# Kernel optimization log

Hardware: AMD Instinct MI355X
Metric: run time of the kernel (lower is better)

## Reference

```python
import jax, jax.numpy as jnp
import numpy as np

B, T, C, H = 8, 1024, 1024, 16
HD = C // H  # head dim = 64
NEG = -1e9


def setup_inputs() -> dict:
    key = jax.random.key(0)
    ks = jax.random.split(key, 10)
    total = B * T
    x = jax.random.normal(ks[0], (total, C), dtype=jnp.float32)
    # identity pack: each padded row is a contiguous chunk of tokens
    padpack_index = jnp.arange(total, dtype=jnp.int64).reshape(B, T)
    # sorted per-row sequence ids -> block-diagonal attention within each packed row
    padpack_batch = jnp.sort(jax.random.randint(ks[1], (B, T), 0, 4, dtype=jnp.int32), axis=-1)
    padpack_inverse_index = jnp.arange(total, dtype=jnp.int64)
    s = 1.0 / np.sqrt(C)
    Wq = jax.random.uniform(ks[2], (C, C), jnp.float32, -s, s)
    bq = jax.random.uniform(ks[3], (C,), jnp.float32, -s, s)
    Wk = jax.random.uniform(ks[4], (C, C), jnp.float32, -s, s)
    bk = jax.random.uniform(ks[5], (C,), jnp.float32, -s, s)
    Wv = jax.random.uniform(ks[6], (C, C), jnp.float32, -s, s)
    bv = jax.random.uniform(ks[7], (C,), jnp.float32, -s, s)
    Wp = jax.random.uniform(ks[8], (C, C), jnp.float32, -s, s)
    bp = jax.random.uniform(ks[9], (C,), jnp.float32, -s, s)
    return {"x": x, "padpack_index": padpack_index, "padpack_batch": padpack_batch,
            "padpack_inverse_index": padpack_inverse_index,
            "Wq": Wq, "bq": bq, "Wk": Wk, "bk": bk, "Wv": Wv, "bv": bv, "Wp": Wp, "bp": bp}


def reference(x, padpack_index, padpack_batch, padpack_inverse_index,
              Wq, bq, Wk, bk, Wv, bv, Wp, bp):
    # gather ragged tokens into padded [B, T, C]
    xp = x[padpack_index]
    # torch Linear: y = x @ W.T + b
    q = (xp @ Wq.T + bq).reshape(B, T, H, HD)
    k = (xp @ Wk.T + bk).reshape(B, T, H, HD)
    v = (xp @ Wv.T + bv).reshape(B, T, H, HD)
    scale = 1.0 / np.sqrt(HD).astype(np.float32)
    att = jnp.einsum('bihd,bjhd->bhij', q, k) * scale  # [B,H,T,T]
    # mask: token pairs from different packed sequences cannot attend
    mask = (padpack_batch[:, :, None] != padpack_batch[:, None, :])[:, None]  # [B,1,T,T]
    att = jnp.where(mask, NEG, att)
    att = jax.nn.softmax(att, axis=-1)
    y = jnp.einsum('bhij,bjhd->bihd', att, v).reshape(B, T, C)
    y = y @ Wp.T + bp
    # scatter back to ragged layout [total_tokens, C]
    return y.reshape(B * T, C)[padpack_inverse_index]
```

## Files before the change

kernel.cpp:

```cpp
#include <hip/hip_runtime.h>


typedef __attribute__((ext_vector_type(8))) short short8;
typedef __attribute__((ext_vector_type(4))) float f32x4;
typedef __attribute__((ext_vector_type(4))) unsigned uint4v;

#define MFMA16(a, b, c) __builtin_amdgcn_mfma_f32_16x16x32_bf16((a), (b), (c), 0, 0, 0)

__device__ __forceinline__ ushort f2b(float f) {
  union { float f; unsigned u; } v; v.f = f;
  unsigned u = v.u;
  return (ushort)((u + 0x7fffu + ((u >> 16) & 1u)) >> 16);
}

__device__ __forceinline__ void gload16(const void* g, void* l) {
  __builtin_amdgcn_global_load_lds((const __attribute__((address_space(1))) unsigned int*)g,
                                   (__attribute__((address_space(3))) unsigned int*)l,
                                   16, 0, 0);
}

__device__ __forceinline__ void cvt4(const float* __restrict__ s, ushort* __restrict__ d) {
  const float4 v = *(const float4*)s;
  ushort4 r; r.x = f2b(v.x); r.y = f2b(v.y); r.z = f2b(v.z); r.w = f2b(v.w);
  *(ushort4*)d = r;
}

__global__ __launch_bounds__(256) void prep(const float* __restrict__ x,
    const float* __restrict__ wq, const float* __restrict__ wk,
    const float* __restrict__ wv, const float* __restrict__ wp,
    ushort* __restrict__ xb, ushort* __restrict__ wb,
    const int* __restrict__ pb, int* __restrict__ bnd) {
  const int bid = blockIdx.x;
  if (bid >= 12288) {
    const int b = bid - 12288;
    const int* p = pb + b * 1024;
    const int i = threadIdx.x;
#pragma unroll
    for (int e = 0; e < 4; ++e) {
      const int idx = i * 4 + e;
      const int cur = p[idx];
      const int prev = (idx == 0) ? -1 : p[idx - 1];
      for (int v = prev + 1; v <= cur; ++v) bnd[b * 8 + v] = idx;
    }
    if (i == 255) {
      const int cur = p[1023];
      for (int v = cur + 1; v <= 4; ++v) bnd[b * 8 + v] = 1024;
    }
    return;
  }
  const long long e0 = ((long long)bid * 256 + threadIdx.x) * 4;
  const long long NX = 8388608ll;
  if (e0 < NX) {
    cvt4(x + e0, xb + e0);
  } else {
    const long long t = e0 - NX;
    const int sel = (int)(t >> 20);
    const float* w = sel == 0 ? wq : sel == 1 ? wk : sel == 2 ? wv : wp;
    cvt4(w + (t & 1048575), wb + t);
  }
}

template <int MODE>
__global__ __launch_bounds__(512, 2) void gemm8(
    const ushort* __restrict__ A, const ushort* __restrict__ Bw,
    const float* __restrict__ bias0, const float* __restrict__ bias1,
    const float* __restrict__ bias2,
    ushort* __restrict__ O0, ushort* __restrict__ O1, ushort* __restrict__ O2,
    float* __restrict__ Of) {
  constexpr int ACH = 256 * 64;
  constexpr int BCH = 128 * 64;
  constexpr int BUFB = 2 * (ACH + BCH);
  __shared__ __align__(16) char smem[3 * BUFB];

  const int tid = threadIdx.x, lane = tid & 63, wid = tid >> 6;
  const int wr = wid >> 1, wc = wid & 1;
  const int lg = lane >> 4, lc = lane & 15;

  const int id = blockIdx.x;
  const int s = id >> 3;
  const int m0 = ((id & 7) * 4 + (s & 3)) << 8;
  const int n0 = (s >> 2) << 7;

  f32x4 acc[4][4] = {};

  const int sr0 = tid >> 2;
  const int sc0 = (tid & 3) ^ ((sr0 >> 1) & 3);

#define STAGE(dst_, kh, kt) { \
    char* ad = (dst_) + (kh) * ACH; \
    char* bd = (dst_) + 2 * ACH + (kh) * BCH; \
    const int kcol = (kt) * 64 + (kh) * 32; \
    gload16(A + (size_t)(m0 + sr0) * 1024 + kcol + sc0 * 8, ad + tid * 16); \
    gload16(A + (size_t)(m0 + 128 + sr0) * 1024 + kcol + sc0 * 8, ad + (tid + 512) * 16); \
    gload16(Bw + (size_t)(n0 + sr0) * 1024 + kcol + sc0 * 8, bd + tid * 16); \
  }

#define PHASE_COMPUTE(src_, kh) { \
    const char* ab = (src_) + (kh) * ACH; \
    const char* bb = (src_) + 2 * ACH + (kh) * BCH; \
    short8 af[4]; short8 bf[4]; \
    _Pragma("unroll") \
    for (int f = 0; f < 4; ++f) { \
      const int row = wr * 64 + f * 16 + lc; \
      af[f] = *(const short8*)(ab + row * 64 + ((lg ^ ((row >> 1) & 3)) << 4)); \
    } \
    _Pragma("unroll") \
    for (int g = 0; g < 4; ++g) { \
      const int row = wc * 64 + g * 16 + lc; \
      bf[g] = *(const short8*)(bb + row * 64 + ((lg ^ ((row >> 1) & 3)) << 4)); \
    } \
    __builtin_amdgcn_s_setprio(1); \
    _Pragma("unroll") \
    for (int f = 0; f < 4; ++f) \
      _Pragma("unroll") \
      for (int g = 0; g < 4; ++g) \
        acc[f][g] = MFMA16(af[f], bf[g], acc[f][g]); \
    __builtin_amdgcn_s_setprio(0); \
  }

#define WAITVM(n) { asm volatile("s_waitcnt vmcnt(" #n ")" ::: "memory"); }
#define BARF() { __builtin_amdgcn_s_barrier(); asm volatile("" ::: "memory"); }

  char* b0 = smem;
  char* b1 = smem + BUFB;
  char* b2 = smem + 2 * BUFB;

  STAGE(b0, 0, 0)
  STAGE(b0, 1, 0)
  STAGE(b1, 0, 1)
  STAGE(b1, 1, 1)

  for (int t = 0; t < 14; ++t) {
    WAITVM(9)
    BARF()
    STAGE(b2, 0, t + 2)
    PHASE_COMPUTE(b0, 0)
    WAITVM(9)
    BARF()
    STAGE(b2, 1, t + 2)
    PHASE_COMPUTE(b0, 1)
    char* tmp = b0; b0 = b1; b1 = b2; b2 = tmp;
  }
  WAITVM(9)
  BARF()
  PHASE_COMPUTE(b0, 0)
  WAITVM(6)
  BARF()
  PHASE_COMPUTE(b0, 1)
  WAITVM(3)
  BARF()
  PHASE_COMPUTE(b1, 0)
  WAITVM(0)
  BARF()
  PHASE_COMPUTE(b1, 1)

  if constexpr (MODE == 0) {
    const int sel = n0 >> 10, nloc = n0 & 1023;
    const float* bias = sel == 0 ? bias0 : sel == 1 ? bias1 : bias2;
    float bval[4];
#pragma unroll
    for (int g = 0; g < 4; ++g) bval[g] = bias[nloc + wc * 64 + g * 16 + lc];
    if (sel < 2) {
      ushort* dst = sel ? O1 : O0;
#pragma unroll
      for (int f = 0; f < 4; ++f)
#pragma unroll
        for (int j = 0; j < 4; ++j) {
          const size_t row = m0 + wr * 64 + f * 16 + lg * 4 + j;
#pragma unroll
          for (int g = 0; g < 4; ++g)
            dst[row * 1024 + nloc + wc * 64 + g * 16 + lc] = f2b(acc[f][g][j] + bval[g]);
        }
    } else {
      ushort (*Ts)[136] = (ushort(*)[136])smem;
#pragma unroll
      for (int mh = 0; mh < 2; ++mh) {
        __syncthreads();
        if ((wr >> 1) == mh) {
#pragma unroll
          for (int f = 0; f < 4; ++f)
#pragma unroll
            for (int g = 0; g < 4; ++g)
#pragma unroll
              for (int j = 0; j < 4; ++j)
                Ts[(wr & 1) * 64 + f * 16 + lg * 4 + j][wc * 64 + g * 16 + lc] =
                    f2b(acc[f][g][j] + bval[g]);
        }
        __syncthreads();
        const int c = tid >> 2;
        const int th = (tid & 3) * 32;
        const int gt = m0 + mh * 128;
        const int b = gt >> 10;
        const int t0 = (gt & 1023) + th;
        const int gc = nloc + c;
        ushort* dp = O2 + ((size_t)((b * 16 + (gc >> 6)) * 64 + (gc & 63))) * 1024 + t0;
#pragma unroll
        for (int gb = 0; gb < 4; ++gb) {
          short8 pk;
#pragma unroll
          for (int u = 0; u < 8; ++u) pk[u] = (short)Ts[th + gb * 8 + u][c];
          *(short8*)(dp + gb * 8) = pk;
        }
      }
    }
  } else {
    float bval[4];
#pragma unroll
    for (int g = 0; g < 4; ++g) bval[g] = bias0[n0 + wc * 64 + g * 16 + lc];
#pragma unroll
    for (int f = 0; f < 4; ++f)
#pragma unroll
      for (int j = 0; j < 4; ++j) {
        const size_t row = m0 + wr * 64 + f * 16 + lg * 4 + j;
#pragma unroll
        for (int g = 0; g < 4; ++g)
          Of[row * 1024 + n0 + wc * 64 + g * 16 + lc] = acc[f][g][j] + bval[g];
      }
  }
#undef STAGE
#undef PHASE_COMPUTE
#undef WAITVM
#undef BARF
}

__global__ __launch_bounds__(512) void attn(const ushort* __restrict__ Q,
    const ushort* __restrict__ K, const ushort* __restrict__ Vt,
    const int* __restrict__ bnd, ushort* __restrict__ O) {
  __shared__ __align__(16) char kvbuf[2][16384];

  const int tid = threadIdx.x, lane = tid & 63;
  const int lg = lane >> 4, lc = lane & 15;

  const int id = blockIdx.x;
  const int xcd = id & 7, slot = id >> 3;
  const int bh = xcd + 8 * (slot >> 3);
  const int qt = slot & 7;
  const int b = bh >> 4, h = bh & 15;
  const int q0 = qt * 128 + (tid >> 6) * 16;

  const int* bd = bnd + b * 8;
  const int b1 = bd[1], b2 = bd[2], b3 = bd[3], b4 = bd[4];
#define SEGID(k) (((k) >= b1) + ((k) >= b2) + ((k) >= b3) + ((k) >= b4))

  const int qid = SEGID(q0 + lc);
  int klo_l = (qid > 0) ? b1 : 0;
  klo_l = (qid > 1) ? b2 : klo_l;
  klo_l = (qid > 2) ? b3 : klo_l;
  int khi_l = (qid > 0) ? b2 : b1;
  khi_l = (qid > 1) ? b3 : khi_l;
  khi_l = (qid > 2) ? b4 : khi_l;

  const int bq_lo = SEGID(qt * 128), bq_hi = SEGID(qt * 128 + 127);
  unsigned am = 0;
#pragma unroll
  for (int jt = 0; jt < 16; ++jt) {
    const int tlo = SEGID(jt * 64), thi = SEGID(jt * 64 + 63);
    if (thi >= bq_lo && tlo <= bq_hi) am |= (1u << jt);
  }

  const ushort* qp = Q + (size_t)(b * 1024 + q0 + lc) * 1024 + h * 64 + lg * 8;
  const short8 qf0 = *(const short8*)qp;
  const short8 qf1 = *(const short8*)(qp + 32);

  const int r0 = tid >> 3;
  const int c16 = (tid & 7) ^ (r0 & 7);
  const ushort* Kg = K + (size_t)(b * 1024 + r0) * 1024 + h * 64 + c16 * 8;
  const ushort* Vg = Vt + (size_t)(bh * 64 + r0) * 1024 + c16 * 8;

#define STAGE(bufp, j) { \
    gload16(Kg + (size_t)(j) * 1024, (bufp) + tid * 16); \
    gload16(Vg + (j), (bufp) + 8192 + tid * 16); }

#define SOFF(r, ch) ((r) * 128 + ((((ch) ^ ((r) & 7))) << 4))

  float mr = -1e30f, lr = 0.f;
  f32x4 o[4] = {};

  unsigned rem = am;
  int jc = __builtin_ctz(rem) * 64;
  rem &= rem - 1;
  STAGE(kvbuf[0], jc)
  __syncthreads();
  int cur = 0;

  const int aA = ((lane & 16) << 3) + ((lane & 15) << 2);
  const int aB = aA + 64;
  const bool hi = (lane & 32) != 0;

  for (;;) {
    int jn = -1;
    if (rem) {
      jn = __builtin_ctz(rem) * 64;
      rem &= rem - 1;
      STAGE(kvbuf[cur ^ 1], jn)
    }
    const char* bufK = kvbuf[cur];
    const char* bufV = kvbuf[cur] + 8192;

    short8 kf[8];
#pragma unroll
    for (int n = 0; n < 4; ++n) {
      const int rr = n * 16 + lc;
      kf[2 * n] = *(const short8*)(bufK + SOFF(rr, lg));
      kf[2 * n + 1] = *(const short8*)(bufK + SOFF(rr, lg + 4));
    }
    f32x4 s[4];
    __builtin_amdgcn_s_setprio(1);
#pragma unroll
    for (int n = 0; n < 4; ++n) {
      f32x4 z = {};
      z = MFMA16(kf[2 * n], qf0, z);
      s[n] = MFMA16(kf[2 * n + 1], qf1, z);
    }
    __builtin_amdgcn_s_setprio(0);

#pragma unroll
    for (int n = 0; n < 4; ++n) {
      const int kk = jc + n * 16 + lg * 4;
#pragma unroll
      for (int r = 0; r < 4; ++r) {
        const bool ok = (kk + r >= klo_l) && (kk + r < khi_l);
        s[n][r] = ok ? s[n][r] * 0.125f : -1e9f;
      }
    }

    float rm = fmaxf(fmaxf(fmaxf(s[0][0], s[0][1]), fmaxf(s[0][2], s[0][3])),
                     fmaxf(fmaxf(fmaxf(s[1][0], s[1][1]), fmaxf(s[1][2], s[1][3])),
                           fmaxf(fmaxf(fmaxf(s[2][0], s[2][1]), fmaxf(s[2][2], s[2][3])),
                                 fmaxf(fmaxf(s[3][0], s[3][1]), fmaxf(s[3][2], s[3][3])))));
    rm = fmaxf(rm, __shfl_xor(rm, 16));
    rm = fmaxf(rm, __shfl_xor(rm, 32));
    float mn = mr;
    if (!__all(rm <= mr + 8.f)) {
      mn = fmaxf(mr, rm);
      const float sf = __expf(mr - mn);
      mr = mn;
      lr *= sf;
      const float s0 = __shfl(sf, lg * 4 + 0);
      const float s1 = __shfl(sf, lg * 4 + 1);
      const float s2 = __shfl(sf, lg * 4 + 2);
      const float s3 = __shfl(sf, lg * 4 + 3);
#pragma unroll
      for (int n = 0; n < 4; ++n) {
        o[n][0] *= s0; o[n][1] *= s1; o[n][2] *= s2; o[n][3] *= s3;
      }
    }
    float rs = 0.f;
#pragma unroll
    for (int n = 0; n < 4; ++n)
#pragma unroll
      for (int r = 0; r < 4; ++r) {
        const float p = __expf(s[n][r] - mn);
        s[n][r] = p; rs += p;
      }
    rs += __shfl_xor(rs, 16);
    rs += __shfl_xor(rs, 32);
    lr += rs;

    unsigned u[4][2];
#pragma unroll
    for (int n = 0; n < 4; ++n) {
      asm("v_cvt_pk_bf16_f32 %0, %1, %2" : "=v"(u[n][0]) : "v"(s[n][0]), "v"(s[n][1]));
      asm("v_cvt_pk_bf16_f32 %0, %1, %2" : "=v"(u[n][1]) : "v"(s[n][2]), "v"(s[n][3]));
    }
    uint4v pwm[2];
#pragma unroll
    for (int m = 0; m < 2; ++m) {
      const unsigned x0 = __builtin_amdgcn_ds_bpermute(aA, u[2 * m][0]);
      const unsigned y0 = __builtin_amdgcn_ds_bpermute(aA, u[2 * m + 1][0]);
      const unsigned x1 = __builtin_amdgcn_ds_bpermute(aA, u[2 * m][1]);
      const unsigned y1 = __builtin_amdgcn_ds_bpermute(aA, u[2 * m + 1][1]);
      const unsigned x2 = __builtin_amdgcn_ds_bpermute(aB, u[2 * m][0]);
      const unsigned y2 = __builtin_amdgcn_ds_bpermute(aB, u[2 * m + 1][0]);
      const unsigned x3 = __builtin_amdgcn_ds_bpermute(aB, u[2 * m][1]);
      const unsigned y3 = __builtin_amdgcn_ds_bpermute(aB, u[2 * m + 1][1]);
      uint4v w;
      w.x = hi ? y0 : x0;
      w.y = hi ? y1 : x1;
      w.z = hi ? y2 : x2;
      w.w = hi ? y3 : x3;
      pwm[m] = w;
    }
    const short8 p0 = *reinterpret_cast<const short8*>(&pwm[0]);
    const short8 p1 = *reinterpret_cast<const short8*>(&pwm[1]);

    short8 vv[8];
#pragma unroll
    for (int n = 0; n < 4; ++n) {
      const int rr = n * 16 + lc;
      vv[2 * n] = *(const short8*)(bufV + SOFF(rr, lg));
      vv[2 * n + 1] = *(const short8*)(bufV + SOFF(rr, lg + 4));
    }
    __builtin_amdgcn_s_setprio(1);
#pragma unroll
    for (int n = 0; n < 4; ++n) {
      o[n] = MFMA16(p0, vv[2 * n], o[n]);
      o[n] = MFMA16(p1, vv[2 * n + 1], o[n]);
    }
    __builtin_amdgcn_s_setprio(0);

    if (jn < 0) break;
    __syncthreads();
    cur ^= 1;
    jc = jn;
  }

  const float linv = 1.f / lr;
  const float i0 = __shfl(linv, lg * 4 + 0);
  const float i1 = __shfl(linv, lg * 4 + 1);
  const float i2 = __shfl(linv, lg * 4 + 2);
  const float i3 = __shfl(linv, lg * 4 + 3);
#pragma unroll
  for (int n = 0; n < 4; ++n) {
    const size_t base = (size_t)(b * 1024 + q0) * 1024 + h * 64 + n * 16 + lc;
    O[base + 0 * 1024 + (size_t)lg * 4096] = f2b(o[n][0] * i0);
    O[base + 1 * 1024 + (size_t)lg * 4096] = f2b(o[n][1] * i1);
    O[base + 2 * 1024 + (size_t)lg * 4096] = f2b(o[n][2] * i2);
    O[base + 3 * 1024 + (size_t)lg * 4096] = f2b(o[n][3] * i3);
  }
#undef STAGE
#undef SOFF
#undef SEGID
}

extern "C" void kernel_launch(void* const* d_in, const int* in_sizes, int n_in,
                              void* d_out, int out_size, void* d_ws, size_t ws_size,
                              hipStream_t stream) {
  const float* x  = (const float*)d_in[0];
  const int*  pb  = (const int*)d_in[2];
  const float* Wq = (const float*)d_in[4]; const float* bq = (const float*)d_in[5];
  const float* Wk = (const float*)d_in[6]; const float* bk = (const float*)d_in[7];
  const float* Wv = (const float*)d_in[8]; const float* bv = (const float*)d_in[9];
  const float* Wp = (const float*)d_in[10]; const float* bp = (const float*)d_in[11];
  float* out = (float*)d_out;
  char* ws = (char*)d_ws;

  ushort* xb = (ushort*)ws;
  ushort* wb = (ushort*)(ws + (16u << 20));
  ushort* Qb = (ushort*)(ws + (24u << 20));
  ushort* Kb = (ushort*)(ws + (40u << 20));
  ushort* Vt = (ushort*)(ws + (56u << 20));
  int*    bnd = (int*)(ws + (72u << 20));
  ushort* Ob = xb;

  prep<<<12296, 256, 0, stream>>>(x, Wq, Wk, Wv, Wp, xb, wb, pb, bnd);
  gemm8<0><<<768, 512, 0, stream>>>(xb, wb, bq, bk, bv, Qb, Kb, Vt, nullptr);
  attn<<<1024, 512, 0, stream>>>(Qb, Kb, Vt, bnd, Ob);
  gemm8<1><<<256, 512, 0, stream>>>(Ob, wb + (3 << 20), bp,
                                    nullptr, nullptr, nullptr, nullptr, nullptr, out);
}
```

Measured before the change: 149.9 us.

## Process two KV tiles per attention loop iteration with larger LDS buffers

The attention kernel now stages and processes two 64-key tiles per loop iteration (128 keys), doubling the LDS double-buffer to 32KB per stage. Online-softmax max/rescale and the barrier happen once per pair of tiles instead of per tile, reducing synchronization and reduction overhead. Invalid second tiles are masked via a validity flag. It costs more LDS (64KB total) and registers, which may reduce occupancy, and odd tile counts waste a masked tile's compute.

After: 152.3 us. Within noise of the previous version (+1.6%).

```diff
diff --git a/kernel.cpp b/kernel.cpp
--- a/kernel.cpp
+++ b/kernel.cpp
@@ -226,7 +226,7 @@
 __global__ __launch_bounds__(512) void attn(const ushort* __restrict__ Q,
     const ushort* __restrict__ K, const ushort* __restrict__ Vt,
     const int* __restrict__ bnd, ushort* __restrict__ O) {
-  __shared__ __align__(16) char kvbuf[2][16384];
+  __shared__ __align__(16) char kvbuf[2][32768];
 
   const int tid = threadIdx.x, lane = tid & 63;
   const int lg = lane >> 4, lc = lane & 15;
@@ -267,7 +267,7 @@
   const ushort* Kg = K + (size_t)(b * 1024 + r0) * 1024 + h * 64 + c16 * 8;
   const ushort* Vg = Vt + (size_t)(bh * 64 + r0) * 1024 + c16 * 8;
 
-#define STAGE(bufp, j) { \
+#define STG1(bufp, j) { \
     gload16(Kg + (size_t)(j) * 1024, (bufp) + tid * 16); \
     gload16(Vg + (j), (bufp) + 8192 + tid * 16); }
 
@@ -277,9 +277,11 @@
   f32x4 o[4] = {};
 
   unsigned rem = am;
-  int jc = __builtin_ctz(rem) * 64;
-  rem &= rem - 1;
-  STAGE(kvbuf[0], jc)
+  int jA = __builtin_ctz(rem) * 64; rem &= rem - 1;
+  int jB = jA; bool vB = false;
+  if (rem) { jB = __builtin_ctz(rem) * 64; rem &= rem - 1; vB = true; }
+  STG1(kvbuf[0], jA)
+  STG1(kvbuf[0] + 16384, jB)
   __syncthreads();
   int cur = 0;
 
@@ -288,46 +290,70 @@
   const bool hi = (lane & 32) != 0;
 
   for (;;) {
-    int jn = -1;
+    int jA2 = -1, jB2 = 0; bool vB2 = false;
     if (rem) {
-      jn = __builtin_ctz(rem) * 64;
-      rem &= rem - 1;
-      STAGE(kvbuf[cur ^ 1], jn)
-    }
-    const char* bufK = kvbuf[cur];
-    const char* bufV = kvbuf[cur] + 8192;
-
-    short8 kf[8];
+      jA2 = __builtin_ctz(rem) * 64; rem &= rem - 1;
+      jB2 = jA2;
+      if (rem) { jB2 = __builtin_ctz(rem) * 64; rem &= rem - 1; vB2 = true; }
+      STG1(kvbuf[cur ^ 1], jA2)
+      STG1(kvbuf[cur ^ 1] + 16384, jB2)
+    }
+    const char* bA = kvbuf[cur];
+    const char* bB = kvbuf[cur] + 16384;
+
+    f32x4 s[8];
+    {
+      short8 kf[8];
+#pragma unroll
+      for (int n = 0; n < 4; ++n) {
+        const int rr = n * 16 + lc;
+        kf[2 * n] = *(const short8*)(bA + SOFF(rr, lg));
+        kf[2 * n + 1] = *(const short8*)(bA + SOFF(rr, lg + 4));
+      }
+      __builtin_amdgcn_s_setprio(1);
+#pragma unroll
+      for (int n = 0; n < 4; ++n) {
+        f32x4 z = {};
+        z = MFMA16(kf[2 * n], qf0, z);
+        s[n] = MFMA16(kf[2 * n + 1], qf1, z);
+      }
+      __builtin_amdgcn_s_setprio(0);
+    }
+    {
+      short8 kf[8];
+#pragma unroll
+      for (int n = 0; n < 4; ++n) {
+        const int rr = n * 16 + lc;
+        kf[2 * n] = *(const short8*)(bB + SOFF(rr, lg));
+        kf[2 * n + 1] = *(const short8*)(bB + SOFF(rr, lg + 4));
+      }
+      __builtin_amdgcn_s_setprio(1);
+#pragma unroll
+      for (int n = 0; n < 4; ++n) {
+        f32x4 z = {};
+        z = MFMA16(kf[2 * n], qf0, z);
+        s[4 + n] = MFMA16(kf[2 * n + 1], qf1, z);
+      }
+      __builtin_amdgcn_s_setprio(0);
+    }
+
 #pragma unroll
     for (int n = 0; n < 4; ++n) {
-      const int rr = n * 16 + lc;
-      kf[2 * n] = *(const short8*)(bufK + SOFF(rr, lg));
-      kf[2 * n + 1] = *(const short8*)(bufK + SOFF(rr, lg + 4));
-    }
-    f32x4 s[4];
-    __builtin_amdgcn_s_setprio(1);
-#pragma unroll
-    for (int n = 0; n < 4; ++n) {
-      f32x4 z = {};
-      z = MFMA16(kf[2 * n], qf0, z);
-      s[n] = MFMA16(kf[2 * n + 1], qf1, z);
-    }
-    __builtin_amdgcn_s_setprio(0);
-
-#pragma unroll
-    for (int n = 0; n < 4; ++n) {
-      const int kk = jc + n * 16 + lg * 4;
+      const int kkA = jA + n * 16 + lg * 4;
+      const int kkB = jB + n * 16 + lg * 4;
 #pragma unroll
       for (int r = 0; r < 4; ++r) {
-        const bool ok = (kk + r >= klo_l) && (kk + r < khi_l);
-        s[n][r] = ok ? s[n][r] * 0.125f : -1e9f;
-      }
-    }
-
-    float rm = fmaxf(fmaxf(fmaxf(s[0][0], s[0][1]), fmaxf(s[0][2], s[0][3])),
-                     fmaxf(fmaxf(fmaxf(s[1][0], s[1][1]), fmaxf(s[1][2], s[1][3])),
-                           fmaxf(fmaxf(fmaxf(s[2][0], s[2][1]), fmaxf(s[2][2], s[2][3])),
-                                 fmaxf(fmaxf(s[3][0], s[3][1]), fmaxf(s[3][2], s[3][3])))));
+        const bool okA = (kkA + r >= klo_l) && (kkA + r < khi_l);
+        s[n][r] = okA ? s[n][r] * 0.125f : -1e9f;
+        const bool okB = vB && (kkB + r >= klo_l) && (kkB + r < khi_l);
+        s[4 + n][r] = okB ? s[4 + n][r] * 0.125f : -1e9f;
+      }
+    }
+
+    float rm = -1e30f;
+#pragma unroll
+    for (int n = 0; n < 8; ++n)
+      rm = fmaxf(rm, fmaxf(fmaxf(s[n][0], s[n][1]), fmaxf(s[n][2], s[n][3])));
     rm = fmaxf(rm, __shfl_xor(rm, 16));
     rm = fmaxf(rm, __shfl_xor(rm, 32));
     float mn = mr;
@@ -347,7 +373,7 @@
     }
     float rs = 0.f;
 #pragma unroll
-    for (int n = 0; n < 4; ++n)
+    for (int n = 0; n < 8; ++n)
 #pragma unroll
       for (int r = 0; r < 4; ++r) {
         const float p = __expf(s[n][r] - mn);
@@ -357,52 +383,56 @@
     rs += __shfl_xor(rs, 32);
     lr += rs;
 
-    unsigned u[4][2];
-#pragma unroll
-    for (int n = 0; n < 4; ++n) {
-      asm("v_cvt_pk_bf16_f32 %0, %1, %2" : "=v"(u[n][0]) : "v"(s[n][0]), "v"(s[n][1]));
-      asm("v_cvt_pk_bf16_f32 %0, %1, %2" : "=v"(u[n][1]) : "v"(s[n][2]), "v"(s[n][3]));
-    }
-    uint4v pwm[2];
-#pragma unroll
-    for (int m = 0; m < 2; ++m) {
-      const unsigned x0 = __builtin_amdgcn_ds_bpermute(aA, u[2 * m][0]);
-      const unsigned y0 = __builtin_amdgcn_ds_bpermute(aA, u[2 * m + 1][0]);
-      const unsigned x1 = __builtin_amdgcn_ds_bpermute(aA, u[2 * m][1]);
-      const unsigned y1 = __builtin_amdgcn_ds_bpermute(aA, u[2 * m + 1][1]);
-      const unsigned x2 = __builtin_amdgcn_ds_bpermute(aB, u[2 * m][0]);
-      const unsigned y2 = __builtin_amdgcn_ds_bpermute(aB, u[2 * m + 1][0]);
-      const unsigned x3 = __builtin_amdgcn_ds_bpermute(aB, u[2 * m][1]);
-      const unsigned y3 = __builtin_amdgcn_ds_bpermute(aB, u[2 * m + 1][1]);
-      uint4v w;
-      w.x = hi ? y0 : x0;
-      w.y = hi ? y1 : x1;
-      w.z = hi ? y2 : x2;
-      w.w = hi ? y3 : x3;
-      pwm[m] = w;
-    }
-    const short8 p0 = *reinterpret_cast<const short8*>(&pwm[0]);
-    const short8 p1 = *reinterpret_cast<const short8*>(&pwm[1]);
-
-    short8 vv[8];
-#pragma unroll
-    for (int n = 0; n < 4; ++n) {
-      const int rr = n * 16 + lc;
-      vv[2 * n] = *(const short8*)(bufV + SOFF(rr, lg));
-      vv[2 * n + 1] = *(const short8*)(bufV + SOFF(rr, lg + 4));
-    }
-    __builtin_amdgcn_s_setprio(1);
-#pragma unroll
-    for (int n = 0; n < 4; ++n) {
-      o[n] = MFMA16(p0, vv[2 * n], o[n]);
-      o[n] = MFMA16(p1, vv[2 * n + 1], o[n]);
-    }
-    __builtin_amdgcn_s_setprio(0);
-
-    if (jn < 0) break;
+#pragma unroll
+    for (int t2 = 0; t2 < 2; ++t2) {
+      unsigned u[4][2];
+#pragma unroll
+      for (int n = 0; n < 4; ++n) {
+        asm("v_cvt_pk_bf16_f32 %0, %1, %2" : "=v"(u[n][0]) : "v"(s[4 * t2 + n][0]), "v"(s[4 * t2 + n][1]));
+        asm("v_cvt_pk_bf16_f32 %0, %1, %2" : "=v"(u[n][1]) : "v"(s[4 * t2 + n][2]), "v"(s[4 * t2 + n][3]));
+      }
+      uint4v pwm[2];
+#pragma unroll
+      for (int m = 0; m < 2; ++m) {
+        const unsigned x0 = __builtin_amdgcn_ds_bpermute(aA, u[2 * m][0]);
+        const unsigned y0 = __builtin_amdgcn_ds_bpermute(aA, u[2 * m + 1][0]);
+        const unsigned x1 = __builtin_amdgcn_ds_bpermute(aA, u[2 * m][1]);
+        const unsigned y1 = __builtin_amdgcn_ds_bpermute(aA, u[2 * m + 1][1]);
+        const unsigned x2 = __builtin_amdgcn_ds_bpermute(aB, u[2 * m][0]);
+        const unsigned y2 = __builtin_amdgcn_ds_bpermute(aB, u[2 * m + 1][0]);
+        const unsigned x3 = __builtin_amdgcn_ds_bpermute(aB, u[2 * m][1]);
+        const unsigned y3 = __builtin_amdgcn_ds_bpermute(aB, u[2 * m + 1][1]);
+        uint4v w;
+        w.x = hi ? y0 : x0;
+        w.y = hi ? y1 : x1;
+        w.z = hi ? y2 : x2;
+        w.w = hi ? y3 : x3;
+        pwm[m] = w;
+      }
+      const short8 p0 = *reinterpret_cast<const short8*>(&pwm[0]);
+      const short8 p1 = *reinterpret_cast<const short8*>(&pwm[1]);
+
+      const char* bufV = (t2 ? bB : bA) + 8192;
+      short8 vv[8];
+#pragma unroll
+      for (int n = 0; n < 4; ++n) {
+        const int rr = n * 16 + lc;
+        vv[2 * n] = *(const short8*)(bufV + SOFF(rr, lg));
+        vv[2 * n + 1] = *(const short8*)(bufV + SOFF(rr, lg + 4));
+      }
+      __builtin_amdgcn_s_setprio(1);
+#pragma unroll
+      for (int n = 0; n < 4; ++n) {
+        o[n] = MFMA16(p0, vv[2 * n], o[n]);
+        o[n] = MFMA16(p1, vv[2 * n + 1], o[n]);
+      }
+      __builtin_amdgcn_s_setprio(0);
+    }
+
+    if (jA2 < 0) break;
     __syncthreads();
     cur ^= 1;
-    jc = jn;
+    jA = jA2; jB = jB2; vB = vB2;
   }
 
   const float linv = 1.f / lr;
@@ -418,7 +448,7 @@
     O[base + 2 * 1024 + (size_t)lg * 4096] = f2b(o[n][2] * i2);
     O[base + 3 * 1024 + (size_t)lg * 4096] = f2b(o[n][3] * i3);
   }
-#undef STAGE
+#undef STG1
 #undef SOFF
 #undef SEGID
 }
```

## Shrink GEMM tiles to 128x128 with 4-wave blocks and single-phase k-steps

Applied to the files above, without the earlier changes.

Replaces the 256x128-tile, 8-wave GEMM with a 128x128-tile, 4-wave GEMM. It uses 32-wide k-steps in a triple-buffered pipeline with 48KB of shared memory, and doubles the grid sizes for both the QKV and output projections. The V-transpose epilogue is simplified to a single pass over the 128-row tile. The goal is more blocks and better occupancy and load balance across CUs, especially for the smaller output projection. In exchange, each loaded byte gets less reuse and global traffic per FLOP goes up.

New measurement: 150.9 us. About the same (+0.7%).

```diff
diff --git a/kernel.cpp b/kernel.cpp
--- a/kernel.cpp
+++ b/kernel.cpp
@@ -61,43 +61,38 @@
 }
 
 template <int MODE>
-__global__ __launch_bounds__(512, 2) void gemm8(
+__global__ __launch_bounds__(256) void gemm4(
     const ushort* __restrict__ A, const ushort* __restrict__ Bw,
     const float* __restrict__ bias0, const float* __restrict__ bias1,
     const float* __restrict__ bias2,
     ushort* __restrict__ O0, ushort* __restrict__ O1, ushort* __restrict__ O2,
     float* __restrict__ Of) {
-  constexpr int ACH = 256 * 64;
-  constexpr int BCH = 128 * 64;
-  constexpr int BUFB = 2 * (ACH + BCH);
-  __shared__ __align__(16) char smem[3 * BUFB];
+  __shared__ __align__(16) char smem[49152];
 
   const int tid = threadIdx.x, lane = tid & 63, wid = tid >> 6;
   const int wr = wid >> 1, wc = wid & 1;
   const int lg = lane >> 4, lc = lane & 15;
 
   const int id = blockIdx.x;
-  const int s = id >> 3;
-  const int m0 = ((id & 7) * 4 + (s & 3)) << 8;
-  const int n0 = (s >> 2) << 7;
+  const int xcd = id & 7, s = id >> 3;
+  const int m0 = (xcd * 8 + (s & 7)) << 7;
+  const int n0 = (s >> 3) << 7;
 
   f32x4 acc[4][4] = {};
 
-  const int sr0 = tid >> 2;
-  const int sc0 = (tid & 3) ^ ((sr0 >> 1) & 3);
-
-#define STAGE(dst_, kh, kt) { \
-    char* ad = (dst_) + (kh) * ACH; \
-    char* bd = (dst_) + 2 * ACH + (kh) * BCH; \
-    const int kcol = (kt) * 64 + (kh) * 32; \
-    gload16(A + (size_t)(m0 + sr0) * 1024 + kcol + sc0 * 8, ad + tid * 16); \
-    gload16(A + (size_t)(m0 + 128 + sr0) * 1024 + kcol + sc0 * 8, ad + (tid + 512) * 16); \
-    gload16(Bw + (size_t)(n0 + sr0) * 1024 + kcol + sc0 * 8, bd + tid * 16); \
-  }
-
-#define PHASE_COMPUTE(src_, kh) { \
-    const char* ab = (src_) + (kh) * ACH; \
-    const char* bb = (src_) + 2 * ACH + (kh) * BCH; \
+  const int sr = tid >> 2;
+  const int sc = (tid & 3) ^ ((sr >> 1) & 3);
+
+#define STAGE(dst_, kt) { \
+    const int kcol = (kt) * 32; \
+    gload16(A + (size_t)(m0 + sr) * 1024 + kcol + sc * 8, (dst_) + tid * 16); \
+    gload16(A + (size_t)(m0 + 64 + sr) * 1024 + kcol + sc * 8, (dst_) + 4096 + tid * 16); \
+    gload16(Bw + (size_t)(n0 + sr) * 1024 + kcol + sc * 8, (dst_) + 8192 + tid * 16); \
+    gload16(Bw + (size_t)(n0 + 64 + sr) * 1024 + kcol + sc * 8, (dst_) + 12288 + tid * 16); }
+
+#define PHASE_COMPUTE(src_) { \
+    const char* ab = (src_); \
+    const char* bb = (src_) + 8192; \
     short8 af[4]; short8 bf[4]; \
     _Pragma("unroll") \
     for (int f = 0; f < 4; ++f) { \
@@ -122,37 +117,25 @@
 #define BARF() { __builtin_amdgcn_s_barrier(); asm volatile("" ::: "memory"); }
 
   char* b0 = smem;
-  char* b1 = smem + BUFB;
-  char* b2 = smem + 2 * BUFB;
-
-  STAGE(b0, 0, 0)
-  STAGE(b0, 1, 0)
-  STAGE(b1, 0, 1)
-  STAGE(b1, 1, 1)
-
-  for (int t = 0; t < 14; ++t) {
-    WAITVM(9)
+  char* b1 = smem + 16384;
+  char* b2 = smem + 32768;
+
+  STAGE(b0, 0)
+  STAGE(b1, 1)
+
+  for (int t = 0; t < 30; ++t) {
+    WAITVM(4)
     BARF()
-    STAGE(b2, 0, t + 2)
-    PHASE_COMPUTE(b0, 0)
-    WAITVM(9)
-    BARF()
-    STAGE(b2, 1, t + 2)
-    PHASE_COMPUTE(b0, 1)
+    STAGE(b2, t + 2)
+    PHASE_COMPUTE(b0)
     char* tmp = b0; b0 = b1; b1 = b2; b2 = tmp;
   }
-  WAITVM(9)
+  WAITVM(4)
   BARF()
-  PHASE_COMPUTE(b0, 0)
-  WAITVM(6)
-  BARF()
-  PHASE_COMPUTE(b0, 1)
-  WAITVM(3)
-  BARF()
-  PHASE_COMPUTE(b1, 0)
+  PHASE_COMPUTE(b0)
   WAITVM(0)
   BARF()
-  PHASE_COMPUTE(b1, 1)
+  PHASE_COMPUTE(b1)
 
   if constexpr (MODE == 0) {
     const int sel = n0 >> 10, nloc = n0 & 1023;
@@ -173,34 +156,28 @@
         }
     } else {
       ushort (*Ts)[136] = (ushort(*)[136])smem;
-#pragma unroll
-      for (int mh = 0; mh < 2; ++mh) {
-        __syncthreads();
-        if ((wr >> 1) == mh) {
-#pragma unroll
-          for (int f = 0; f < 4; ++f)
-#pragma unroll
-            for (int g = 0; g < 4; ++g)
-#pragma unroll
-              for (int j = 0; j < 4; ++j)
-                Ts[(wr & 1) * 64 + f * 16 + lg * 4 + j][wc * 64 + g * 16 + lc] =
-                    f2b(acc[f][g][j] + bval[g]);
-        }
-        __syncthreads();
-        const int c = tid >> 2;
-        const int th = (tid & 3) * 32;
-        const int gt = m0 + mh * 128;
-        const int b = gt >> 10;
-        const int t0 = (gt & 1023) + th;
-        const int gc = nloc + c;
-        ushort* dp = O2 + ((size_t)((b * 16 + (gc >> 6)) * 64 + (gc & 63))) * 1024 + t0;
-#pragma unroll
-        for (int gb = 0; gb < 4; ++gb) {
-          short8 pk;
-#pragma unroll
-          for (int u = 0; u < 8; ++u) pk[u] = (short)Ts[th + gb * 8 + u][c];
-          *(short8*)(dp + gb * 8) = pk;
-        }
+      __syncthreads();
+#pragma unroll
+      for (int f = 0; f < 4; ++f)
+#pragma unroll
+        for (int g = 0; g < 4; ++g)
+#pragma unroll
+          for (int j = 0; j < 4; ++j)
+            Ts[wr * 64 + f * 16 + lg * 4 + j][wc * 64 + g * 16 + lc] =
+                f2b(acc[f][g][j] + bval[g]);
+      __syncthreads();
+      const int c = tid >> 1;
+      const int th = (tid & 1) * 64;
+      const int gc = nloc + c;
+      const int gt = m0 + th;
+      const int b = gt >> 10, t = gt & 1023;
+      ushort* dp = O2 + ((size_t)((b * 16 + (gc >> 6)) * 64 + (gc & 63))) * 1024 + t;
+#pragma unroll
+      for (int gb = 0; gb < 8; ++gb) {
+        short8 pk;
+#pragma unroll
+        for (int u = 0; u < 8; ++u) pk[u] = (short)Ts[th + gb * 8 + u][c];
+        *(short8*)(dp + gb * 8) = pk;
       }
     }
   } else {
@@ -444,8 +421,8 @@
   ushort* Ob = xb;
 
   prep<<<12296, 256, 0, stream>>>(x, Wq, Wk, Wv, Wp, xb, wb, pb, bnd);
-  gemm8<0><<<768, 512, 0, stream>>>(xb, wb, bq, bk, bv, Qb, Kb, Vt, nullptr);
+  gemm4<0><<<1536, 256, 0, stream>>>(xb, wb, bq, bk, bv, Qb, Kb, Vt, nullptr);
   attn<<<1024, 512, 0, stream>>>(Qb, Kb, Vt, bnd, Ob);
-  gemm8<1><<<256, 512, 0, stream>>>(Ob, wb + (3 << 20), bp,
+  gemm4<1><<<512, 256, 0, stream>>>(Ob, wb + (3 << 20), bp,
                                     nullptr, nullptr, nullptr, nullptr, nullptr, out);
 }
```
